# Kernel optimization log

Hardware: AMD Instinct MI355X
Metric: run time of the kernel (lower is better)

Reference implementation:

```python
import jax, jax.numpy as jnp
import numpy as np
import math

B, S, HID, NH, HD = 2, 1024, 768, 12, 64
MAXP = 1024  # max_position_embeddings


def setup_inputs() -> dict:
    key = jax.random.key(0)
    ks = jax.random.split(key, 12)
    s = 0.02
    return {
        "hidden_states": jax.random.normal(ks[0], (B, S, HID), jnp.float32),
        "attention_mask": jnp.zeros((B, 1, 1, S), jnp.float32),
        "scaled_attention_mask": jax.random.uniform(ks[1], (1, 1, S, S), dtype=jnp.float32),
        "selector_outputs": jax.random.uniform(ks[2], (B, 1, S, 1), dtype=jnp.float32),
        "Wq": jax.random.normal(ks[3], (HID, HID), jnp.float32) * s,
        "bq": jnp.zeros((HID,), jnp.float32),
        "Wk": jax.random.normal(ks[4], (HID, HID), jnp.float32) * s,
        "bk": jnp.zeros((HID,), jnp.float32),
        "Wv": jax.random.normal(ks[5], (HID, HID), jnp.float32) * s,
        "bv": jnp.zeros((HID,), jnp.float32),
        "dist_emb": jax.random.normal(ks[6], (2 * MAXP - 1, HD), jnp.float32) * s,
    }


def _heads(x):
    # [B,S,HID] -> [B,NH,S,HD]
    return x.reshape(B, S, NH, HD).transpose(0, 2, 1, 3)


def reference(hidden_states, attention_mask, scaled_attention_mask, selector_outputs,
              Wq, bq, Wk, bk, Wv, bv, dist_emb):
    q = _heads(hidden_states @ Wq + bq)  # [B,NH,S,HD]
    k = _heads(hidden_states @ Wk + bk)
    v = _heads(hidden_states @ Wv + bv)

    scores = jnp.einsum('bhld,bhrd->bhlr', q, k)  # [B,NH,S,S]

    # relative_key positional bias
    pos = jnp.arange(S)
    dist_idx = pos[:, None] - pos[None, :] + (MAXP - 1)  # [S,S] in [0, 2*MAXP-2]
    pos_emb = dist_emb[dist_idx]  # [S,S,HD]
    scores = scores + jnp.einsum('bhld,lrd->bhlr', q, pos_emb)

    scores = scores / math.sqrt(HD)
    scores = scores + attention_mask  # additive mask (global branch)

    probs = jax.nn.softmax(scores, axis=-1)  # dropout prob = 0.0 -> identity
    context = jnp.einsum('bhlr,bhrd->bhld', probs, v)

    # local (selector-gated) branch; note: attention_mask added a second time,
    # faithful to the original code
    scores_l = scores * scaled_attention_mask + attention_mask
    probs_l = jax.nn.softmax(scores_l, axis=-1)
    local_context = jnp.einsum('bhlr,bhrd->bhld', probs_l, v)

    sel = selector_outputs  # [B,1,S,1]
    context = sel * local_context + (1.0 - sel) * context  # [B,NH,S,HD]

    # [B,NH,S,HD] -> [B,S,HID]
    return context.transpose(0, 2, 1, 3).reshape(B, S, HID)
```

## Files before the change

### kernel.cpp

```cpp
#include <hip/hip_runtime.h>
#include <hip/hip_bf16.h>
#include <math.h>

#define BB   2
#define SS   1024
#define HIDD 768
#define NHH  12
#define HDD  64

typedef float f32x4 __attribute__((ext_vector_type(4)));
typedef short bf8   __attribute__((ext_vector_type(8)));
typedef unsigned short u16;
typedef u16 u16x8 __attribute__((ext_vector_type(8)));
typedef u16 u16x4 __attribute__((ext_vector_type(4)));

__device__ __forceinline__ u16 f2bf(float x) {
  unsigned int u = __float_as_uint(x);
  u += 0x7fffu + ((u >> 16) & 1u);
  return (u16)(u >> 16);
}

__device__ __forceinline__ bf8 ldfrag(const u16* t, int row, int kc) {
  return *(const bf8*)&t[row * 64 + (kc ^ ((row & 7) << 3))];
}

__global__ __launch_bounds__(256) void xconv_kernel(const float* __restrict__ X,
                                                    u16* __restrict__ Xb) {
  int i = (blockIdx.x * 256 + threadIdx.x) * 8;
  float4 a = *(const float4*)&X[i];
  float4 b = *(const float4*)&X[i + 4];
  u16x8 o;
  o[0] = f2bf(a.x); o[1] = f2bf(a.y); o[2] = f2bf(a.z); o[3] = f2bf(a.w);
  o[4] = f2bf(b.x); o[5] = f2bf(b.y); o[6] = f2bf(b.z); o[7] = f2bf(b.w);
  *(u16x8*)&Xb[i] = o;
}

__global__ __launch_bounds__(256) void wtconv_kernel(
    const float* __restrict__ Wq, const float* __restrict__ Wk,
    const float* __restrict__ Wv, u16* __restrict__ Wt) {
  const int zi = blockIdx.z;
  const float* __restrict__ W = (zi == 0) ? Wq : (zi == 1 ? Wk : Wv);
  const int n0 = blockIdx.x * 64;
  const int k0 = blockIdx.y * 64;
  __shared__ float t[64][65];
  const int tid = threadIdx.x;
  {
    const int kl = tid >> 4;
    const int nl = (tid & 15) * 4;
#pragma unroll
    for (int p = 0; p < 4; ++p) {
      float4 v = *(const float4*)&W[(size_t)(k0 + kl + 16 * p) * HIDD + n0 + nl];
      t[kl + 16 * p][nl + 0] = v.x;
      t[kl + 16 * p][nl + 1] = v.y;
      t[kl + 16 * p][nl + 2] = v.z;
      t[kl + 16 * p][nl + 3] = v.w;
    }
  }
  __syncthreads();
  {
    const int nl = tid >> 4;
    const int cl = (tid & 15) * 4;
#pragma unroll
    for (int p = 0; p < 4; ++p) {
      const int n = nl + 16 * p;
      u16x4 o;
      o[0] = f2bf(t[cl + 0][n]);
      o[1] = f2bf(t[cl + 1][n]);
      o[2] = f2bf(t[cl + 2][n]);
      o[3] = f2bf(t[cl + 3][n]);
      *(u16x4*)&Wt[(size_t)(zi * HIDD + n0 + n) * HIDD + k0 + cl] = o;
    }
  }
}

__global__ __launch_bounds__(256) void econv_kernel(const float* __restrict__ demb,
                                                    u16* __restrict__ eb) {
  int i = (blockIdx.x * 256 + threadIdx.x) * 8;
  if (i < 2047 * HDD) {
    float4 a = *(const float4*)&demb[i];
    float4 b = *(const float4*)&demb[i + 4];
    u16x8 o;
    o[0] = f2bf(a.x); o[1] = f2bf(a.y); o[2] = f2bf(a.z); o[3] = f2bf(a.w);
    o[4] = f2bf(b.x); o[5] = f2bf(b.y); o[6] = f2bf(b.z); o[7] = f2bf(b.w);
    *(u16x8*)&eb[i] = o;
  }
}

__global__ __launch_bounds__(256) void qkv_mfma_kernel(
    const u16* __restrict__ Xb,
    const u16* __restrict__ Wt,
    const float* __restrict__ bq, const float* __restrict__ bk,
    const float* __restrict__ bv,
    u16* __restrict__ qb, u16* __restrict__ kb, u16* __restrict__ vt) {
  const int bn = blockIdx.x;
  const int bm = blockIdx.y;
  const int zi = bn / 6;

  __shared__ u16 As[64 * 64];
  __shared__ u16 Bs[128 * 64];

  const int tid  = threadIdx.x;
  const int lane = tid & 63;
  const int w    = tid >> 6;
  const int g    = lane >> 4;
  const int ln   = lane & 15;
  const int wm   = (w >> 1) * 32;
  const int wn   = (w & 1) * 64;

  f32x4 acc[2][4] = {};

  const int srow = tid >> 3;
  const int scol = (tid & 7) * 8;
  const u16* Ag = Xb + (size_t)(bm * 64 + srow) * HIDD + scol;
  const u16* Bg = Wt + (size_t)(bn * 128 + srow) * HIDD + scol;

  for (int k0 = 0; k0 < HIDD; k0 += 64) {
    if (k0) __syncthreads();
#pragma unroll
    for (int p = 0; p < 2; ++p) {
      const int r = srow + 32 * p;
      const int sw = (r & 7) << 3;
      *(u16x8*)&As[r * 64 + (scol ^ sw)] =
          *(const u16x8*)&Ag[(size_t)(32 * p) * HIDD + k0];
    }
#pragma unroll
    for (int p = 0; p < 4; ++p) {
      const int r = srow + 32 * p;
      const int sw = (r & 7) << 3;
      *(u16x8*)&Bs[r * 64 + (scol ^ sw)] =
          *(const u16x8*)&Bg[(size_t)(32 * p) * HIDD + k0];
    }
    __syncthreads();

    bf8 af[2][2], bfr[4][2];
#pragma unroll
    for (int f = 0; f < 2; ++f)
#pragma unroll
      for (int kk = 0; kk < 2; ++kk)
        af[f][kk] = ldfrag(As, wm + 16 * f + ln, kk * 32 + g * 8);
#pragma unroll
    for (int f = 0; f < 4; ++f)
#pragma unroll
      for (int kk = 0; kk < 2; ++kk)
        bfr[f][kk] = ldfrag(Bs, wn + 16 * f + ln, kk * 32 + g * 8);
    if (zi < 2) {
#pragma unroll
      for (int mf = 0; mf < 2; ++mf)
#pragma unroll
        for (int nf = 0; nf < 4; ++nf)
#pragma unroll
          for (int kk = 0; kk < 2; ++kk)
            acc[mf][nf] = __builtin_amdgcn_mfma_f32_16x16x32_bf16(
                bfr[nf][kk], af[mf][kk], acc[mf][nf], 0, 0, 0);
    } else {
#pragma unroll
      for (int mf = 0; mf < 2; ++mf)
#pragma unroll
        for (int nf = 0; nf < 4; ++nf)
#pragma unroll
          for (int kk = 0; kk < 2; ++kk)
            acc[mf][nf] = __builtin_amdgcn_mfma_f32_16x16x32_bf16(
                af[mf][kk], bfr[nf][kk], acc[mf][nf], 0, 0, 0);
    }
  }

  const int mrow  = bm * 64 + wm;
  const int nbase = (bn % 6) * 128 + wn;
  const int h     = nbase >> 6;

  if (zi < 2) {
    const float* __restrict__ bias = zi ? bk : bq;
    u16* __restrict__ outp = zi ? kb : qb;
#pragma unroll
    for (int nf = 0; nf < 4; ++nf) {
      const int d0 = 16 * nf + 4 * g;
      float4 bi = *(const float4*)&bias[nbase + d0];
#pragma unroll
      for (int mf = 0; mf < 2; ++mf) {
        const int m = mrow + 16 * mf + ln;
        const int b = m >> 10, s = m & 1023;
        u16x4 o;
        o[0] = f2bf(acc[mf][nf][0] + bi.x);
        o[1] = f2bf(acc[mf][nf][1] + bi.y);
        o[2] = f2bf(acc[mf][nf][2] + bi.z);
        o[3] = f2bf(acc[mf][nf][3] + bi.w);
        *(u16x4*)&outp[(((size_t)(b * NHH + h)) * SS + s) * HDD + d0] = o;
      }
    }
  } else {
#pragma unroll
    for (int nf = 0; nf < 4; ++nf) {
      const int d = 16 * nf + ln;
      const float bi = bv[nbase + d];
#pragma unroll
      for (int mf = 0; mf < 2; ++mf) {
        const int m = mrow + 16 * mf + 4 * g;
        const int b = m >> 10, s = m & 1023;
        u16x4 o;
        o[0] = f2bf(acc[mf][nf][0] + bi);
        o[1] = f2bf(acc[mf][nf][1] + bi);
        o[2] = f2bf(acc[mf][nf][2] + bi);
        o[3] = f2bf(acc[mf][nf][3] + bi);
        *(u16x4*)&vt[(((size_t)(b * NHH + h)) * HDD + d) * SS + s] = o;
      }
    }
  }
}

__global__ __launch_bounds__(256) void attn_kernel(
    const u16* __restrict__ qbg,
    const u16* __restrict__ kbg,
    const u16* __restrict__ vtg,
    const u16* __restrict__ eb,
    const float* __restrict__ am,
    const float* __restrict__ smask,
    const float* __restrict__ selp,
    float* __restrict__ out) {
  const int l0 = blockIdx.x * 32;
  const int h  = blockIdx.y;
  const int b  = blockIdx.z;
  const int bh = b * NHH + h;
  const size_t hoff = (size_t)bh * SS * HDD;

  __shared__ __align__(16) u16 smbuf[24576];
  u16* ks  = smbuf;
  u16* vs  = smbuf + 8192;
  u16* ps1 = smbuf + 16384;
  u16* ps2 = smbuf + 20480;

  const int tid  = threadIdx.x;
  const int lane = tid & 63;
  const int w    = tid >> 6;
  const int p    = w >> 1;
  const int wp   = w & 1;
  const int g    = lane >> 4;
  const int ln   = lane & 15;

  bf8 qf[2];
  {
    const u16* qp = qbg + hoff + (size_t)(l0 + 16 * wp + ln) * HDD + g * 8;
    qf[0] = *(const bf8*)(qp);
    qf[1] = *(const bf8*)(qp + 32);
  }

  f32x4 acc1[4] = {}, acc2[4] = {};
  float m1[4], m2[4], sum1[4], sum2[4];
#pragma unroll
  for (int i = 0; i < 4; ++i) {
    m1[i] = -INFINITY; m2[i] = -INFINITY; sum1[i] = 0.f; sum2[i] = 0.f;
  }

  const int tid128 = tid & 127;
  const int rr = tid128 >> 2;
  const int cc = (tid128 & 3) << 4;
  u16* ksw = ks + p * 4096;
  u16* vsw = vs + p * 4096;
  u16* p1w = ps1 + w * 1024;
  u16* p2w = ps2 + w * 1024;

  for (int t = 0; t < 8; ++t) {
    const int r0 = 512 * p + 64 * t;
    __syncthreads();
    {
      const u16* kgp = kbg + hoff + (size_t)r0 * HDD;
      const u16* vgp = vtg + hoff + r0;
#pragma unroll
      for (int pp = 0; pp < 2; ++pp) {
        const int r = rr + 32 * pp;
        const int sw = (r & 7) << 3;
        u16x8 a0 = *(const u16x8*)&kgp[(size_t)r * HDD + cc];
        u16x8 a1 = *(const u16x8*)&kgp[(size_t)r * HDD + cc + 8];
        *(u16x8*)&ksw[r * 64 + (cc ^ sw)] = a0;
        *(u16x8*)&ksw[r * 64 + ((cc + 8) ^ sw)] = a1;
        u16x8 c0 = *(const u16x8*)&vgp[(size_t)r * SS + cc];
        u16x8 c1 = *(const u16x8*)&vgp[(size_t)r * SS + cc + 8];
        *(u16x8*)&vsw[r * 64 + (cc ^ sw)] = c0;
        *(u16x8*)&vsw[r * 64 + ((cc + 8) ^ sw)] = c1;
      }
    }
    float amv[4], smv[4][4];
#pragma unroll
    for (int ct = 0; ct < 4; ++ct) {
      amv[ct] = am[(b << 10) + r0 + 16 * ct + ln];
#pragma unroll
      for (int i = 0; i < 4; ++i)
        smv[ct][i] =
            smask[(size_t)(l0 + 16 * wp + 4 * g + i) * SS + r0 + 16 * ct + ln];
    }
    __syncthreads();

    f32x4 sc[4];
    __builtin_amdgcn_s_setprio(1);
#pragma unroll
    for (int ct = 0; ct < 4; ++ct) {
      f32x4 x = {0.f, 0.f, 0.f, 0.f};
#pragma unroll
      for (int kk = 0; kk < 2; ++kk)
        x = __builtin_amdgcn_mfma_f32_16x16x32_bf16(
            qf[kk], ldfrag(ksw, ct * 16 + ln, kk * 32 + g * 8), x, 0, 0, 0);
      sc[ct] = x;
    }

    const int ebase = l0 - r0 + 960 + 16 * wp;
    f32x4 x5[5];
#pragma unroll
    for (int c5 = 0; c5 < 5; ++c5) {
      const int gr = min(max(ebase + c5 * 16 + ln, 0), 2046);
      const u16* ep = eb + (size_t)gr * HDD + g * 8;
      f32x4 x = {0.f, 0.f, 0.f, 0.f};
      x = __builtin_amdgcn_mfma_f32_16x16x32_bf16(qf[0], *(const bf8*)ep, x, 0, 0, 0);
      x = __builtin_amdgcn_mfma_f32_16x16x32_bf16(qf[1], *(const bf8*)(ep + 32), x, 0, 0, 0);
      x5[c5] = x;
    }
    __builtin_amdgcn_s_setprio(0);

#pragma unroll
    for (int i = 0; i < 4; ++i) {
      const int ll = 4 * g + i;
      const int srcIdx = (lane & 48) | ((ll + 15 - ln) & 15);
      const float y0 = __shfl(x5[0][i], srcIdx, 64);
      const float y1 = __shfl(x5[1][i], srcIdx, 64);
      const float y2 = __shfl(x5[2][i], srcIdx, 64);
      const float y3 = __shfl(x5[3][i], srcIdx, 64);
      const float y4 = __shfl(x5[4][i], srcIdx, 64);
      const bool hi = ln < ll;
      float tb[4];
      tb[0] = hi ? y4 : y3;
      tb[1] = hi ? y3 : y2;
      tb[2] = hi ? y2 : y1;
      tb[3] = hi ? y1 : y0;

      float s1r[4], s2r[4];
#pragma unroll
      for (int ct = 0; ct < 4; ++ct) {
        const float s1 = (sc[ct][i] + tb[ct]) * 0.125f + amv[ct];
        s1r[ct] = s1;
        s2r[ct] = s1 * smv[ct][i] + amv[ct];
      }
      {
        float mx = fmaxf(fmaxf(s1r[0], s1r[1]), fmaxf(s1r[2], s1r[3]));
#pragma unroll
        for (int off = 1; off < 16; off <<= 1) mx = fmaxf(mx, __shfl_xor(mx, off, 64));
        const float mn = fmaxf(m1[i], mx);
        const float scale = __expf(m1[i] - mn);
        float rs = 0.f;
#pragma unroll
        for (int ct = 0; ct < 4; ++ct) {
          const float pr = __expf(s1r[ct] - mn);
          const int c = 16 * ct + ln;
          p1w[ll * 64 + (c ^ ((ll & 7) << 3))] = f2bf(pr);
          rs += pr;
        }
#pragma unroll
        for (int off = 1; off < 16; off <<= 1) rs += __shfl_xor(rs, off, 64);
        sum1[i] = sum1[i] * scale + rs;
        m1[i] = mn;
#pragma unroll
        for (int dt = 0; dt < 4; ++dt) acc1[dt][i] *= scale;
      }
      {
        float mx = fmaxf(fmaxf(s2r[0], s2r[1]), fmaxf(s2r[2], s2r[3]));
#pragma unroll
        for (int off = 1; off < 16; off <<= 1) mx = fmaxf(mx, __shfl_xor(mx, off, 64));
        const float mn = fmaxf(m2[i], mx);
        const float scale = __expf(m2[i] - mn);
        float rs = 0.f;
#pragma unroll
        for (int ct = 0; ct < 4; ++ct) {
          const float pr = __expf(s2r[ct] - mn);
          const int c = 16 * ct + ln;
          p2w[ll * 64 + (c ^ ((ll & 7) << 3))] = f2bf(pr);
          rs += pr;
        }
#pragma unroll
        for (int off = 1; off < 16; off <<= 1) rs += __shfl_xor(rs, off, 64);
        sum2[i] = sum2[i] * scale + rs;
        m2[i] = mn;
#pragma unroll
        for (int dt = 0; dt < 4; ++dt) acc2[dt][i] *= scale;
      }
    }

    __builtin_amdgcn_s_setprio(1);
#pragma unroll
    for (int kk = 0; kk < 2; ++kk) {
      bf8 pa = ldfrag(p1w, ln, kk * 32 + g * 8);
      bf8 pb = ldfrag(p2w, ln, kk * 32 + g * 8);
#pragma unroll
      for (int dt = 0; dt < 4; ++dt) {
        bf8 vb = ldfrag(vsw, dt * 16 + ln, kk * 32 + g * 8);
        acc1[dt] = __builtin_amdgcn_mfma_f32_16x16x32_bf16(pa, vb, acc1[dt], 0, 0, 0);
        acc2[dt] = __builtin_amdgcn_mfma_f32_16x16x32_bf16(pb, vb, acc2[dt], 0, 0, 0);
      }
    }
    __builtin_amdgcn_s_setprio(0);
  }

  __syncthreads();
  float* scr = (float*)smbuf;
  if (p == 1) {
#pragma unroll
    for (int i = 0; i < 4; ++i) {
      const int row = 4 * g + i;
#pragma unroll
      for (int dt = 0; dt < 4; ++dt) {
        scr[wp * 1024 + row * 64 + dt * 16 + ln] = acc1[dt][i];
        scr[2048 + wp * 1024 + row * 64 + dt * 16 + ln] = acc2[dt][i];
      }
      if (ln == 0) {
        const int sb = 4096 + (wp * 16 + row) * 4;
        scr[sb + 0] = m1[i];
        scr[sb + 1] = sum1[i];
        scr[sb + 2] = m2[i];
        scr[sb + 3] = sum2[i];
      }
    }
  }
  __syncthreads();
  if (p == 0) {
#pragma unroll
    for (int i = 0; i < 4; ++i) {
      const int row = 4 * g + i;
      const int lg  = l0 + 16 * wp + row;
      const int sb  = 4096 + (wp * 16 + row) * 4;
      const float mB1 = scr[sb + 0], sB1 = scr[sb + 1];
      const float mB2 = scr[sb + 2], sB2 = scr[sb + 3];
      const float M1 = fmaxf(m1[i], mB1);
      const float e1A = __expf(m1[i] - M1), e1B = __expf(mB1 - M1);
      const float inv1 = 1.f / (sum1[i] * e1A + sB1 * e1B);
      const float M2 = fmaxf(m2[i], mB2);
      const float e2A = __expf(m2[i] - M2), e2B = __expf(mB2 - M2);
      const float inv2 = 1.f / (sum2[i] * e2A + sB2 * e2B);
      const float se = selp[(b << 10) + lg];
#pragma unroll
      for (int dt = 0; dt < 4; ++dt) {
        const float aB1 = scr[wp * 1024 + row * 64 + dt * 16 + ln];
        const float aB2 = scr[2048 + wp * 1024 + row * 64 + dt * 16 + ln];
        const float o1 = (acc1[dt][i] * e1A + aB1 * e1B) * inv1;
        const float o2 = (acc2[dt][i] * e2A + aB2 * e2B) * inv2;
        out[((size_t)((b << 10) + lg)) * HIDD + h * HDD + dt * 16 + ln] =
            se * o2 + (1.f - se) * o1;
      }
    }
  }
}

extern "C" void kernel_launch(void* const* d_in, const int* in_sizes, int n_in,
                              void* d_out, int out_size, void* d_ws, size_t ws_size,
                              hipStream_t stream) {
  const float* hidden = (const float*)d_in[0];
  const float* am     = (const float*)d_in[1];
  const float* smask  = (const float*)d_in[2];
  const float* selp   = (const float*)d_in[3];
  const float* Wq     = (const float*)d_in[4];
  const float* bq     = (const float*)d_in[5];
  const float* Wk     = (const float*)d_in[6];
  const float* bk     = (const float*)d_in[7];
  const float* Wv     = (const float*)d_in[8];
  const float* bv     = (const float*)d_in[9];
  const float* demb   = (const float*)d_in[10];
  float* out = (float*)d_out;

  u16* wsp = (u16*)d_ws;
  const size_t NEL = (size_t)BB * NHH * SS * HDD;
  u16* Xb  = wsp;
  u16* Wt  = Xb + (size_t)2048 * HIDD;
  u16* qbw = Wt + (size_t)3 * HIDD * HIDD;
  u16* kbw = qbw + NEL;
  u16* vtw = kbw + NEL;
  u16* ebw = vtw + NEL;

  xconv_kernel<<<768, 256, 0, stream>>>(hidden, Xb);
  dim3 gw(HIDD / 64, HIDD / 64, 3);
  wtconv_kernel<<<gw, 256, 0, stream>>>(Wq, Wk, Wv, Wt);
  econv_kernel<<<64, 256, 0, stream>>>(demb, ebw);

  dim3 g1(18, 32);
  qkv_mfma_kernel<<<g1, 256, 0, stream>>>(Xb, Wt, bq, bk, bv, qbw, kbw, vtw);

  dim3 g2(SS / 32, NHH, BB);
  attn_kernel<<<g2, 256, 0, stream>>>(qbw, kbw, vtw, ebw, am, smask, selp, out);
}
```

Before: 105.5 us.

## Transpose score MFMAs so softmax rows reduce in-lane and P stays in registers

Measured after the change: 102.0 us. 1.03x faster.

```diff
diff --git a/kernel.cpp b/kernel.cpp
--- a/kernel.cpp
+++ b/kernel.cpp
@@ -11,6 +11,7 @@
 typedef float f32x4 __attribute__((ext_vector_type(4)));
 typedef short bf8   __attribute__((ext_vector_type(8)));
 typedef unsigned short u16;
+typedef unsigned int u32;
 typedef u16 u16x8 __attribute__((ext_vector_type(8)));
 typedef u16 u16x4 __attribute__((ext_vector_type(4)));
 
@@ -18,6 +19,9 @@
   unsigned int u = __float_as_uint(x);
   u += 0x7fffu + ((u >> 16) & 1u);
   return (u16)(u >> 16);
+}
+__device__ __forceinline__ float bf2f(u16 x) {
+  return __uint_as_float(((u32)x) << 16);
 }
 
 __device__ __forceinline__ bf8 ldfrag(const u16* t, int row, int kc) {
@@ -207,7 +211,7 @@
   }
 }
 
-__global__ __launch_bounds__(256) void attn_kernel(
+__global__ __launch_bounds__(256, 3) void attn_kernel(
     const u16* __restrict__ qbg,
     const u16* __restrict__ kbg,
     const u16* __restrict__ vtg,
@@ -222,11 +226,8 @@
   const int bh = b * NHH + h;
   const size_t hoff = (size_t)bh * SS * HDD;
 
-  __shared__ __align__(16) u16 smbuf[24576];
-  u16* ks  = smbuf;
-  u16* vs  = smbuf + 8192;
-  u16* ps1 = smbuf + 16384;
-  u16* ps2 = smbuf + 20480;
+  __shared__ __align__(16) u16 smbuf[16384];
+  __shared__ __align__(4)  u16 tbuf[4 * 80 * 17];
 
   const int tid  = threadIdx.x;
   const int lane = tid & 63;
@@ -236,6 +237,10 @@
   const int g    = lane >> 4;
   const int ln   = lane & 15;
 
+  u16* ksw = smbuf + p * 4096;
+  u16* vsw = smbuf + 8192 + p * 4096;
+  u16* Tw  = tbuf + w * (80 * 17);
+
   bf8 qf[2];
   {
     const u16* qp = qbg + hoff + (size_t)(l0 + 16 * wp + ln) * HDD + g * 8;
@@ -244,23 +249,35 @@
   }
 
   f32x4 acc1[4] = {}, acc2[4] = {};
-  float m1[4], m2[4], sum1[4], sum2[4];
-#pragma unroll
-  for (int i = 0; i < 4; ++i) {
-    m1[i] = -INFINITY; m2[i] = -INFINITY; sum1[i] = 0.f; sum2[i] = 0.f;
-  }
+  float m1 = -INFINITY, m2 = -INFINITY, sum1 = 0.f, sum2 = 0.f;
 
   const int tid128 = tid & 127;
   const int rr = tid128 >> 2;
   const int cc = (tid128 & 3) << 4;
-  u16* ksw = ks + p * 4096;
-  u16* vsw = vs + p * 4096;
-  u16* p1w = ps1 + w * 1024;
-  u16* p2w = ps2 + w * 1024;
+  const int S0i = ((lane & 16) << 1) | ln;
+  const int S1i = S0i + 16;
+  const bool ghi = (lane & 32) != 0;
 
   for (int t = 0; t < 8; ++t) {
     const int r0 = 512 * p + 64 * t;
     __syncthreads();
+
+    const int W0 = l0 + 16 * wp - r0 + 960;
+    bf8 ef[5][2];
+#pragma unroll
+    for (int c5 = 0; c5 < 5; ++c5) {
+      const int gr = min(W0 + 16 * c5 + ln, 2046);
+      const u16* ep = eb + (size_t)gr * HDD + g * 8;
+      ef[c5][0] = *(const bf8*)(ep);
+      ef[c5][1] = *(const bf8*)(ep + 32);
+    }
+    f32x4 amv[4], smv[4];
+#pragma unroll
+    for (int ct = 0; ct < 4; ++ct) {
+      amv[ct] = *(const f32x4*)&am[(b << 10) + r0 + 16 * ct + 4 * g];
+      smv[ct] = *(const f32x4*)&smask[(size_t)(l0 + 16 * wp + ln) * SS +
+                                      r0 + 16 * ct + 4 * g];
+    }
     {
       const u16* kgp = kbg + hoff + (size_t)r0 * HDD;
       const u16* vgp = vtg + hoff + r0;
@@ -278,119 +295,156 @@
         *(u16x8*)&vsw[r * 64 + ((cc + 8) ^ sw)] = c1;
       }
     }
-    float amv[4], smv[4][4];
-#pragma unroll
-    for (int ct = 0; ct < 4; ++ct) {
-      amv[ct] = am[(b << 10) + r0 + 16 * ct + ln];
+    __syncthreads();
+
+    __builtin_amdgcn_s_setprio(1);
+#pragma unroll
+    for (int c5 = 0; c5 < 5; ++c5) {
+      f32x4 x = {0.f, 0.f, 0.f, 0.f};
+      x = __builtin_amdgcn_mfma_f32_16x16x32_bf16(ef[c5][0], qf[0], x, 0, 0, 0);
+      x = __builtin_amdgcn_mfma_f32_16x16x32_bf16(ef[c5][1], qf[1], x, 0, 0, 0);
 #pragma unroll
       for (int i = 0; i < 4; ++i)
-        smv[ct][i] =
-            smask[(size_t)(l0 + 16 * wp + 4 * g + i) * SS + r0 + 16 * ct + ln];
-    }
-    __syncthreads();
-
+        Tw[(16 * c5 + 4 * g + i) * 17 + ln] = f2bf(x[i]);
+    }
     f32x4 sc[4];
-    __builtin_amdgcn_s_setprio(1);
 #pragma unroll
     for (int ct = 0; ct < 4; ++ct) {
       f32x4 x = {0.f, 0.f, 0.f, 0.f};
 #pragma unroll
       for (int kk = 0; kk < 2; ++kk)
         x = __builtin_amdgcn_mfma_f32_16x16x32_bf16(
-            qf[kk], ldfrag(ksw, ct * 16 + ln, kk * 32 + g * 8), x, 0, 0, 0);
+            ldfrag(ksw, ct * 16 + ln, kk * 32 + g * 8), qf[kk], x, 0, 0, 0);
       sc[ct] = x;
     }
-
-    const int ebase = l0 - r0 + 960 + 16 * wp;
-    f32x4 x5[5];
-#pragma unroll
-    for (int c5 = 0; c5 < 5; ++c5) {
-      const int gr = min(max(ebase + c5 * 16 + ln, 0), 2046);
-      const u16* ep = eb + (size_t)gr * HDD + g * 8;
-      f32x4 x = {0.f, 0.f, 0.f, 0.f};
-      x = __builtin_amdgcn_mfma_f32_16x16x32_bf16(qf[0], *(const bf8*)ep, x, 0, 0, 0);
-      x = __builtin_amdgcn_mfma_f32_16x16x32_bf16(qf[1], *(const bf8*)(ep + 32), x, 0, 0, 0);
-      x5[c5] = x;
-    }
     __builtin_amdgcn_s_setprio(0);
 
-#pragma unroll
-    for (int i = 0; i < 4; ++i) {
-      const int ll = 4 * g + i;
-      const int srcIdx = (lane & 48) | ((ll + 15 - ln) & 15);
-      const float y0 = __shfl(x5[0][i], srcIdx, 64);
-      const float y1 = __shfl(x5[1][i], srcIdx, 64);
-      const float y2 = __shfl(x5[2][i], srcIdx, 64);
-      const float y3 = __shfl(x5[3][i], srcIdx, 64);
-      const float y4 = __shfl(x5[4][i], srcIdx, 64);
-      const bool hi = ln < ll;
-      float tb[4];
-      tb[0] = hi ? y4 : y3;
-      tb[1] = hi ? y3 : y2;
-      tb[2] = hi ? y2 : y1;
-      tb[3] = hi ? y1 : y0;
-
-      float s1r[4], s2r[4];
+    float s1r[4][4], s2r[4][4];
+#pragma unroll
+    for (int ct = 0; ct < 4; ++ct)
+#pragma unroll
+      for (int i = 0; i < 4; ++i) {
+        const int e = ln + 63 - 16 * ct - 4 * g - i;
+        const float tb = bf2f(Tw[e * 17 + ln]);
+        const float s1 = (sc[ct][i] + tb) * 0.125f + amv[ct][i];
+        s1r[ct][i] = s1;
+        s2r[ct][i] = s1 * smv[ct][i] + amv[ct][i];
+      }
+
+    bf8 pa1[2], pa2[2];
+    {
+      float mx = s1r[0][0];
+#pragma unroll
+      for (int ct = 0; ct < 4; ++ct)
+#pragma unroll
+        for (int i = 0; i < 4; ++i) mx = fmaxf(mx, s1r[ct][i]);
+      mx = fmaxf(mx, __shfl_xor(mx, 16, 64));
+      mx = fmaxf(mx, __shfl_xor(mx, 32, 64));
+      const float mn = fmaxf(m1, mx);
+      const float scl = __expf(m1 - mn);
+      m1 = mn;
+      float rs = 0.f;
+      u32 pk[4][2];
 #pragma unroll
       for (int ct = 0; ct < 4; ++ct) {
-        const float s1 = (sc[ct][i] + tb[ct]) * 0.125f + amv[ct];
-        s1r[ct] = s1;
-        s2r[ct] = s1 * smv[ct][i] + amv[ct];
-      }
-      {
-        float mx = fmaxf(fmaxf(s1r[0], s1r[1]), fmaxf(s1r[2], s1r[3]));
-#pragma unroll
-        for (int off = 1; off < 16; off <<= 1) mx = fmaxf(mx, __shfl_xor(mx, off, 64));
-        const float mn = fmaxf(m1[i], mx);
-        const float scale = __expf(m1[i] - mn);
-        float rs = 0.f;
-#pragma unroll
-        for (int ct = 0; ct < 4; ++ct) {
-          const float pr = __expf(s1r[ct] - mn);
-          const int c = 16 * ct + ln;
-          p1w[ll * 64 + (c ^ ((ll & 7) << 3))] = f2bf(pr);
-          rs += pr;
-        }
-#pragma unroll
-        for (int off = 1; off < 16; off <<= 1) rs += __shfl_xor(rs, off, 64);
-        sum1[i] = sum1[i] * scale + rs;
-        m1[i] = mn;
-#pragma unroll
-        for (int dt = 0; dt < 4; ++dt) acc1[dt][i] *= scale;
-      }
-      {
-        float mx = fmaxf(fmaxf(s2r[0], s2r[1]), fmaxf(s2r[2], s2r[3]));
-#pragma unroll
-        for (int off = 1; off < 16; off <<= 1) mx = fmaxf(mx, __shfl_xor(mx, off, 64));
-        const float mn = fmaxf(m2[i], mx);
-        const float scale = __expf(m2[i] - mn);
-        float rs = 0.f;
-#pragma unroll
-        for (int ct = 0; ct < 4; ++ct) {
-          const float pr = __expf(s2r[ct] - mn);
-          const int c = 16 * ct + ln;
-          p2w[ll * 64 + (c ^ ((ll & 7) << 3))] = f2bf(pr);
-          rs += pr;
-        }
-#pragma unroll
-        for (int off = 1; off < 16; off <<= 1) rs += __shfl_xor(rs, off, 64);
-        sum2[i] = sum2[i] * scale + rs;
-        m2[i] = mn;
-#pragma unroll
-        for (int dt = 0; dt < 4; ++dt) acc2[dt][i] *= scale;
+        const float p0 = __expf(s1r[ct][0] - mn);
+        const float p1 = __expf(s1r[ct][1] - mn);
+        const float p2 = __expf(s1r[ct][2] - mn);
+        const float p3 = __expf(s1r[ct][3] - mn);
+        rs += (p0 + p1) + (p2 + p3);
+        pk[ct][0] = (u32)f2bf(p0) | ((u32)f2bf(p1) << 16);
+        pk[ct][1] = (u32)f2bf(p2) | ((u32)f2bf(p3) << 16);
+      }
+      rs += __shfl_xor(rs, 16, 64);
+      rs += __shfl_xor(rs, 32, 64);
+      sum1 = sum1 * scl + rs;
+#pragma unroll
+      for (int i = 0; i < 4; ++i) {
+        const float s = __shfl(scl, (lane & 48) + 4 * g + i, 64);
+#pragma unroll
+        for (int dt = 0; dt < 4; ++dt) acc1[dt][i] *= s;
+      }
+#pragma unroll
+      for (int kk = 0; kk < 2; ++kk) {
+        union { u32 u[4]; bf8 v; } f;
+        const int cA = 2 * kk, cB = 2 * kk + 1;
+        u32 a, bb;
+        a = (u32)__shfl((int)pk[cA][0], S0i, 64);
+        bb = (u32)__shfl((int)pk[cB][0], S0i, 64);
+        f.u[0] = ghi ? bb : a;
+        a = (u32)__shfl((int)pk[cA][1], S0i, 64);
+        bb = (u32)__shfl((int)pk[cB][1], S0i, 64);
+        f.u[1] = ghi ? bb : a;
+        a = (u32)__shfl((int)pk[cA][0], S1i, 64);
+        bb = (u32)__shfl((int)pk[cB][0], S1i, 64);
+        f.u[2] = ghi ? bb : a;
+        a = (u32)__shfl((int)pk[cA][1], S1i, 64);
+        bb = (u32)__shfl((int)pk[cB][1], S1i, 64);
+        f.u[3] = ghi ? bb : a;
+        pa1[kk] = f.v;
+      }
+    }
+    {
+      float mx = s2r[0][0];
+#pragma unroll
+      for (int ct = 0; ct < 4; ++ct)
+#pragma unroll
+        for (int i = 0; i < 4; ++i) mx = fmaxf(mx, s2r[ct][i]);
+      mx = fmaxf(mx, __shfl_xor(mx, 16, 64));
+      mx = fmaxf(mx, __shfl_xor(mx, 32, 64));
+      const float mn = fmaxf(m2, mx);
+      const float scl = __expf(m2 - mn);
+      m2 = mn;
+      float rs = 0.f;
+      u32 pk[4][2];
+#pragma unroll
+      for (int ct = 0; ct < 4; ++ct) {
+        const float p0 = __expf(s2r[ct][0] - mn);
+        const float p1 = __expf(s2r[ct][1] - mn);
+        const float p2 = __expf(s2r[ct][2] - mn);
+        const float p3 = __expf(s2r[ct][3] - mn);
+        rs += (p0 + p1) + (p2 + p3);
+        pk[ct][0] = (u32)f2bf(p0) | ((u32)f2bf(p1) << 16);
+        pk[ct][1] = (u32)f2bf(p2) | ((u32)f2bf(p3) << 16);
+      }
+      rs += __shfl_xor(rs, 16, 64);
+      rs += __shfl_xor(rs, 32, 64);
+      sum2 = sum2 * scl + rs;
+#pragma unroll
+      for (int i = 0; i < 4; ++i) {
+        const float s = __shfl(scl, (lane & 48) + 4 * g + i, 64);
+#pragma unroll
+        for (int dt = 0; dt < 4; ++dt) acc2[dt][i] *= s;
+      }
+#pragma unroll
+      for (int kk = 0; kk < 2; ++kk) {
+        union { u32 u[4]; bf8 v; } f;
+        const int cA = 2 * kk, cB = 2 * kk + 1;
+        u32 a, bb;
+        a = (u32)__shfl((int)pk[cA][0], S0i, 64);
+        bb = (u32)__shfl((int)pk[cB][0], S0i, 64);
+        f.u[0] = ghi ? bb : a;
+        a = (u32)__shfl((int)pk[cA][1], S0i, 64);
+        bb = (u32)__shfl((int)pk[cB][1], S0i, 64);
+        f.u[1] = ghi ? bb : a;
+        a = (u32)__shfl((int)pk[cA][0], S1i, 64);
+        bb = (u32)__shfl((int)pk[cB][0], S1i, 64);
+        f.u[2] = ghi ? bb : a;
+        a = (u32)__shfl((int)pk[cA][1], S1i, 64);
+        bb = (u32)__shfl((int)pk[cB][1], S1i, 64);
+        f.u[3] = ghi ? bb : a;
+        pa2[kk] = f.v;
       }
     }
 
     __builtin_amdgcn_s_setprio(1);
 #pragma unroll
     for (int kk = 0; kk < 2; ++kk) {
-      bf8 pa = ldfrag(p1w, ln, kk * 32 + g * 8);
-      bf8 pb = ldfrag(p2w, ln, kk * 32 + g * 8);
 #pragma unroll
       for (int dt = 0; dt < 4; ++dt) {
         bf8 vb = ldfrag(vsw, dt * 16 + ln, kk * 32 + g * 8);
-        acc1[dt] = __builtin_amdgcn_mfma_f32_16x16x32_bf16(pa, vb, acc1[dt], 0, 0, 0);
-        acc2[dt] = __builtin_amdgcn_mfma_f32_16x16x32_bf16(pb, vb, acc2[dt], 0, 0, 0);
+        acc1[dt] = __builtin_amdgcn_mfma_f32_16x16x32_bf16(pa1[kk], vb, acc1[dt], 0, 0, 0);
+        acc2[dt] = __builtin_amdgcn_mfma_f32_16x16x32_bf16(pa2[kk], vb, acc2[dt], 0, 0, 0);
       }
     }
     __builtin_amdgcn_s_setprio(0);
@@ -407,37 +461,42 @@
         scr[wp * 1024 + row * 64 + dt * 16 + ln] = acc1[dt][i];
         scr[2048 + wp * 1024 + row * 64 + dt * 16 + ln] = acc2[dt][i];
       }
-      if (ln == 0) {
-        const int sb = 4096 + (wp * 16 + row) * 4;
-        scr[sb + 0] = m1[i];
-        scr[sb + 1] = sum1[i];
-        scr[sb + 2] = m2[i];
-        scr[sb + 3] = sum2[i];
-      }
+    }
+    if (g == 0) {
+      const int sb = 4096 + (wp * 16 + ln) * 4;
+      scr[sb + 0] = m1;
+      scr[sb + 1] = sum1;
+      scr[sb + 2] = m2;
+      scr[sb + 3] = sum2;
     }
   }
   __syncthreads();
   if (p == 0) {
+    const int sb = 4096 + (wp * 16 + ln) * 4;
+    const float mB1 = scr[sb + 0], sB1 = scr[sb + 1];
+    const float mB2 = scr[sb + 2], sB2 = scr[sb + 3];
+    const float M1 = fmaxf(m1, mB1);
+    const float e1A = __expf(m1 - M1), e1B = __expf(mB1 - M1);
+    const float inv1 = 1.f / (sum1 * e1A + sB1 * e1B);
+    const float a1 = e1A * inv1, c1 = e1B * inv1;
+    const float M2 = fmaxf(m2, mB2);
+    const float e2A = __expf(m2 - M2), e2B = __expf(mB2 - M2);
+    const float inv2 = 1.f / (sum2 * e2A + sB2 * e2B);
+    const float a2 = e2A * inv2, c2 = e2B * inv2;
 #pragma unroll
     for (int i = 0; i < 4; ++i) {
+      const int src = (lane & 48) + 4 * g + i;
+      const float a1s = __shfl(a1, src, 64), c1s = __shfl(c1, src, 64);
+      const float a2s = __shfl(a2, src, 64), c2s = __shfl(c2, src, 64);
       const int row = 4 * g + i;
-      const int lg  = l0 + 16 * wp + row;
-      const int sb  = 4096 + (wp * 16 + row) * 4;
-      const float mB1 = scr[sb + 0], sB1 = scr[sb + 1];
-      const float mB2 = scr[sb + 2], sB2 = scr[sb + 3];
-      const float M1 = fmaxf(m1[i], mB1);
-      const float e1A = __expf(m1[i] - M1), e1B = __expf(mB1 - M1);
-      const float inv1 = 1.f / (sum1[i] * e1A + sB1 * e1B);
-      const float M2 = fmaxf(m2[i], mB2);
-      const float e2A = __expf(m2[i] - M2), e2B = __expf(mB2 - M2);
-      const float inv2 = 1.f / (sum2[i] * e2A + sB2 * e2B);
+      const int lg = l0 + 16 * wp + row;
       const float se = selp[(b << 10) + lg];
 #pragma unroll
       for (int dt = 0; dt < 4; ++dt) {
         const float aB1 = scr[wp * 1024 + row * 64 + dt * 16 + ln];
         const float aB2 = scr[2048 + wp * 1024 + row * 64 + dt * 16 + ln];
-        const float o1 = (acc1[dt][i] * e1A + aB1 * e1B) * inv1;
-        const float o2 = (acc2[dt][i] * e2A + aB2 * e2B) * inv2;
+        const float o1 = acc1[dt][i] * a1s + aB1 * c1s;
+        const float o2 = acc2[dt][i] * a2s + aB2 * c2s;
         out[((size_t)((b << 10) + lg)) * HIDD + h * HDD + dt * 16 + ln] =
             se * o2 + (1.f - se) * o1;
       }
```
